# Optimization experiments

Measured on AMD Instinct MI355X. Metric: run time of the kernel, lower is better.

## Reference

```python
import jax, jax.numpy as jnp
import numpy as np

LN_EPS = 1e-5
B, T, D, H, NB, HH = 256, 128, 512, 1024, 64, 8


def _layernorm(x, g, b):
    m = x.mean(-1, keepdims=True)
    v = ((x - m) ** 2).mean(-1, keepdims=True)
    return (x - m) / jnp.sqrt(v + LN_EPS) * g + b


def setup_inputs() -> dict:
    key = jax.random.key(0)
    ks = jax.random.split(key, 10)
    init = lambda k, shape, fan: jax.random.normal(k, shape, jnp.float32) * np.float32(1.0 / np.sqrt(fan))
    return {
        "context_features": jax.random.normal(ks[0], (B, T, D), jnp.float32),
        "beam_history": jax.random.randint(ks[1], (B, HH), 0, NB),
        "beam_embed": init(ks[2], (NB, D), D),
        "W_in": init(ks[3], (H, 2 * D), 2 * D), "b_in": jnp.zeros((H,), jnp.float32),
        "W_init": init(ks[4], (H, 2 * D), 2 * D), "b_init": jnp.zeros((H,), jnp.float32),
        "W_ih": init(ks[5], (3 * H, H), H), "b_ih": jnp.zeros((3 * H,), jnp.float32),
        "W_hh": init(ks[6], (3 * H, H), H), "b_hh": jnp.zeros((3 * H,), jnp.float32),
        "ln_g": jnp.ones((H,), jnp.float32), "ln_b": jnp.zeros((H,), jnp.float32),
        "W_o1": init(ks[7], (H, H + D), H + D), "b_o1": jnp.zeros((H,), jnp.float32),
        "W_o2": init(ks[8], (NB, H), H), "b_o2": jnp.zeros((NB,), jnp.float32),
    }


def reference(context_features, beam_history, beam_embed, W_in, b_in, W_init, b_init,
              W_ih, b_ih, W_hh, b_hh, ln_g, ln_b, W_o1, b_o1, W_o2, b_o2):
    # --- init: history embedding mean + global context mean -> initial GRU state ---
    prev0 = beam_history[:, -1]                      # (B,)
    hist_emb = beam_embed[beam_history].mean(axis=1)  # (B, D)
    ctx_global = context_features.mean(axis=1)        # (B, D)
    h0 = jnp.tanh(jnp.concatenate([ctx_global, hist_emb], axis=-1) @ W_init.T + b_init)  # (B, H)

    def step(carry, ctx_t):
        h, prev = carry
        prev_emb = beam_embed[prev]                                            # (B, D)
        x = jax.nn.relu(jnp.concatenate([ctx_t, prev_emb], -1) @ W_in.T + b_in)  # (B, H)
        # PyTorch GRUCell: gate order r, z, n
        gx = x @ W_ih.T + b_ih
        gh = h @ W_hh.T + b_hh
        xr, xz, xn = jnp.split(gx, 3, axis=-1)
        hr, hz, hn = jnp.split(gh, 3, axis=-1)
        r = jax.nn.sigmoid(xr + hr)
        z = jax.nn.sigmoid(xz + hz)
        n = jnp.tanh(xn + r * hn)
        h_new = (1.0 - z) * n + z * h
        h_norm = _layernorm(h_new, ln_g, ln_b)
        o = jax.nn.relu(jnp.concatenate([h_norm, ctx_t], -1) @ W_o1.T + b_o1)
        logits_t = o @ W_o2.T + b_o2                                            # (B, NB)
        pred_next = jnp.argmax(logits_t, axis=-1)
        return (h_new, pred_next), logits_t

    ctx_tbd = jnp.swapaxes(context_features, 0, 1)  # (T, B, D)
    (_, _), logits = jax.lax.scan(step, (h0, prev0), ctx_tbd)
    return jnp.swapaxes(logits, 0, 1)  # (B, T, NB) == ar_logits
```

## Files before the change

### kernel.cpp

```cpp
#include <hip/hip_runtime.h>
#include <hip/hip_bf16.h>


#define TS 68
#define LDPA 40
constexpr int SZ = 262144;
constexpr int TT = 128;
constexpr int LDA_CTX = 65536;

typedef __attribute__((ext_vector_type(8))) short short8_t;
typedef __attribute__((ext_vector_type(4))) float f32x4;


__device__ __forceinline__ unsigned short f2bf_rne(float v) {
    unsigned u = __float_as_uint(v);
    unsigned r = u + 0x7fffu + ((u >> 16) & 1u);
    return (unsigned short)(r >> 16);
}
__device__ __forceinline__ float bfbits2f(unsigned short h) {
    return __uint_as_float(((unsigned)h) << 16);
}
__device__ __forceinline__ void split2(float v, unsigned short& h, unsigned short& l) {
    h = f2bf_rne(v);
    l = f2bf_rne(v - bfbits2f(h));
}
__device__ __forceinline__ void splitA8(const float4& v0, const float4& v1,
                                        short8_t& hi, short8_t& lo) {
    unsigned short h[8], l[8];
    split2(v0.x, h[0], l[0]); split2(v0.y, h[1], l[1]);
    split2(v0.z, h[2], l[2]); split2(v0.w, h[3], l[3]);
    split2(v1.x, h[4], l[4]); split2(v1.y, h[5], l[5]);
    split2(v1.z, h[6], l[6]); split2(v1.w, h[7], l[7]);
    hi = short8_t{(short)h[0],(short)h[1],(short)h[2],(short)h[3],
                  (short)h[4],(short)h[5],(short)h[6],(short)h[7]};
    lo = short8_t{(short)l[0],(short)l[1],(short)l[2],(short)l[3],
                  (short)l[4],(short)l[5],(short)l[6],(short)l[7]};
}


__device__ __forceinline__ void core13b(
    const unsigned short* __restrict__ Ah, const unsigned short* __restrict__ Al,
    int lda, int b0,
    const unsigned short* __restrict__ BhP, const unsigned short* __restrict__ BlP,
    int nKs, int ksbase, int nfb,
    int nIter, unsigned short* sm, f32x4 acc[2][4])
{
    const int tid = threadIdx.x, lane = tid & 63, wid = tid >> 6;
    const int wr = wid >> 1, wc = wid & 1;
    const int l15 = lane & 15, kg = (lane >> 4) * 8;
    const int arow = tid >> 2, acol = (tid & 3) * 8;

    const int ALO = 2560, BUF = 5120;

    const unsigned short* gAh = Ah + (size_t)(b0 + arow) * lda + ksbase * 32 + acol;
    const unsigned short* gAl = Al + (size_t)(b0 + arow) * lda + ksbase * 32 + acol;
    const unsigned short* pBh[4];
    const unsigned short* pBl[4];
#pragma unroll
    for (int ni = 0; ni < 4; ++ni) {
        pBh[ni] = BhP + ((size_t)(nfb + ni) * nKs + ksbase) * 512 + lane * 8;
        pBl[ni] = BlP + ((size_t)(nfb + ni) * nKs + ksbase) * 512 + lane * 8;
    }

    short8_t cBh[4], cBl[4], nBh[4], nBl[4];
    {
        short8_t a_h = *(const short8_t*)gAh;
        short8_t a_l = *(const short8_t*)gAl;
        *(short8_t*)&sm[arow * LDPA + acol]       = a_h;
        *(short8_t*)&sm[ALO + arow * LDPA + acol] = a_l;
#pragma unroll
        for (int ni = 0; ni < 4; ++ni) {
            cBh[ni] = *(const short8_t*)pBh[ni];
            cBl[ni] = *(const short8_t*)pBl[ni];
        }
    }
    __syncthreads();

    int cur = 0;
    const int aro = (wr * 32 + l15) * LDPA + kg;
    for (int i = 0; i < nIter; ++i) {
        short8_t a_h, a_l;
        if (i + 1 < nIter) {
            const int ko = (i + 1) * 32;
            a_h = *(const short8_t*)(gAh + ko);
            a_l = *(const short8_t*)(gAl + ko);
            const size_t fo = (size_t)(i + 1) * 512;
#pragma unroll
            for (int ni = 0; ni < 4; ++ni) {
                nBh[ni] = *(const short8_t*)(pBh[ni] + fo);
                nBl[ni] = *(const short8_t*)(pBl[ni] + fo);
            }
        }
        const unsigned short* S = sm + cur * BUF;
        short8_t afh[2], afl[2];
#pragma unroll
        for (int mi = 0; mi < 2; ++mi) {
            afh[mi] = *(const short8_t*)&S[aro + mi * 16 * LDPA];
            afl[mi] = *(const short8_t*)&S[ALO + aro + mi * 16 * LDPA];
        }
#pragma unroll
        for (int ni = 0; ni < 4; ++ni) {
#pragma unroll
            for (int mi = 0; mi < 2; ++mi) {
                acc[mi][ni] = __builtin_amdgcn_mfma_f32_16x16x32_bf16(afh[mi], cBh[ni], acc[mi][ni], 0, 0, 0);
                acc[mi][ni] = __builtin_amdgcn_mfma_f32_16x16x32_bf16(afh[mi], cBl[ni], acc[mi][ni], 0, 0, 0);
                acc[mi][ni] = __builtin_amdgcn_mfma_f32_16x16x32_bf16(afl[mi], cBh[ni], acc[mi][ni], 0, 0, 0);
            }
        }
        if (i + 1 < nIter) {
            unsigned short* N_ = sm + (cur ^ 1) * BUF;
            *(short8_t*)&N_[arow * LDPA + acol]       = a_h;
            *(short8_t*)&N_[ALO + arow * LDPA + acol] = a_l;
        }
        __syncthreads();
        cur ^= 1;
#pragma unroll
        for (int ni = 0; ni < 4; ++ni) { cBh[ni] = nBh[ni]; cBl[ni] = nBl[ni]; }
    }
}


__device__ __forceinline__ void mfma_core9(
    const float* __restrict__ A, int lda, int b0,
    const unsigned short* __restrict__ Bh, const unsigned short* __restrict__ Bl,
    int ldb, int n0, int k0base, int nIter,
    unsigned short* sm, f32x4 acc[2][4])
{
    const int tid = threadIdx.x, lane = tid & 63, wid = tid >> 6;
    const int wr = wid >> 1, wc = wid & 1;
    const int l15 = lane & 15, kg = (lane >> 4) * 8;
    const int arow = tid >> 2, acol = (tid & 3) * 8;
    const int brow = tid >> 1, bcol = (tid & 1) * 16;

    const int AOFF = 2560, BHOFF = 5120, BLOFF = 10240, BUF = 15360;

    const float* gA = A + (size_t)(b0 + arow) * lda + k0base + acol;
    const unsigned short* gBh = Bh + (size_t)(n0 + brow) * ldb + k0base + bcol;
    const unsigned short* gBl = Bl + (size_t)(n0 + brow) * ldb + k0base + bcol;

    {
        float4 a0 = *(const float4*)gA;
        float4 a1 = *(const float4*)(gA + 4);
        short8_t ah, al;
        splitA8(a0, a1, ah, al);
        short8_t bh0 = *(const short8_t*)gBh;
        short8_t bh1 = *(const short8_t*)(gBh + 8);
        short8_t bl0 = *(const short8_t*)gBl;
        short8_t bl1 = *(const short8_t*)(gBl + 8);
        *(short8_t*)&sm[arow * LDPA + acol]              = ah;
        *(short8_t*)&sm[AOFF + arow * LDPA + acol]       = al;
        *(short8_t*)&sm[BHOFF + brow * LDPA + bcol]      = bh0;
        *(short8_t*)&sm[BHOFF + brow * LDPA + bcol + 8]  = bh1;
        *(short8_t*)&sm[BLOFF + brow * LDPA + bcol]      = bl0;
        *(short8_t*)&sm[BLOFF + brow * LDPA + bcol + 8]  = bl1;
    }
    __syncthreads();

    int cur = 0;
    const int aro = (wr * 32 + l15) * LDPA + kg;
    for (int i = 0; i < nIter; ++i) {
        float4 a0, a1;
        short8_t bh0, bh1, bl0, bl1;
        if (i + 1 < nIter) {
            const int ko = (i + 1) * 32;
            a0 = *(const float4*)(gA + ko);
            a1 = *(const float4*)(gA + ko + 4);
            bh0 = *(const short8_t*)(gBh + ko);
            bh1 = *(const short8_t*)(gBh + ko + 8);
            bl0 = *(const short8_t*)(gBl + ko);
            bl1 = *(const short8_t*)(gBl + ko + 8);
        }
        const unsigned short* S = sm + cur * BUF;
        short8_t afh[2], afl[2];
#pragma unroll
        for (int mi = 0; mi < 2; ++mi) {
            afh[mi] = *(const short8_t*)&S[aro + mi * 16 * LDPA];
            afl[mi] = *(const short8_t*)&S[AOFF + aro + mi * 16 * LDPA];
        }
#pragma unroll
        for (int ni = 0; ni < 4; ++ni) {
            const int bro = (wc * 64 + ni * 16 + l15) * LDPA + kg;
            short8_t b_h = *(const short8_t*)&S[BHOFF + bro];
            short8_t b_l = *(const short8_t*)&S[BLOFF + bro];
#pragma unroll
            for (int mi = 0; mi < 2; ++mi) {
                acc[mi][ni] = __builtin_amdgcn_mfma_f32_16x16x32_bf16(afh[mi], b_h, acc[mi][ni], 0, 0, 0);
                acc[mi][ni] = __builtin_amdgcn_mfma_f32_16x16x32_bf16(afh[mi], b_l, acc[mi][ni], 0, 0, 0);
                acc[mi][ni] = __builtin_amdgcn_mfma_f32_16x16x32_bf16(afl[mi], b_h, acc[mi][ni], 0, 0, 0);
            }
        }
        if (i + 1 < nIter) {
            short8_t ah, al;
            splitA8(a0, a1, ah, al);
            unsigned short* N_ = sm + (cur ^ 1) * BUF;
            *(short8_t*)&N_[arow * LDPA + acol]             = ah;
            *(short8_t*)&N_[AOFF + arow * LDPA + acol]      = al;
            *(short8_t*)&N_[BHOFF + brow * LDPA + bcol]     = bh0;
            *(short8_t*)&N_[BHOFF + brow * LDPA + bcol + 8] = bh1;
            *(short8_t*)&N_[BLOFF + brow * LDPA + bcol]     = bl0;
            *(short8_t*)&N_[BLOFF + brow * LDPA + bcol + 8] = bl1;
        }
        __syncthreads();
        cur ^= 1;
    }
}


__device__ __forceinline__ void gemm_tile64(
    const float* __restrict__ A, int lda, int Mlim, int b0,
    const float* __restrict__ W, int ldw, int n0, int K,
    float* At, float* Wt, float acc[4][4])
{
    const int tid = threadIdx.x;
    const int tx = tid & 15, ty = tid >> 4;
    const int r = tid >> 2, c0 = (tid & 3) << 2;
    for (int k0 = 0; k0 < K; k0 += 16) {
        float4 av = make_float4(0.f, 0.f, 0.f, 0.f);
        if (b0 + r < Mlim)
            av = *(const float4*)(A + (size_t)(b0 + r) * lda + k0 + c0);
        float4 wv = *(const float4*)(W + (size_t)(n0 + r) * ldw + k0 + c0);
        __syncthreads();
        At[(c0+0)*TS + r] = av.x; At[(c0+1)*TS + r] = av.y;
        At[(c0+2)*TS + r] = av.z; At[(c0+3)*TS + r] = av.w;
        Wt[(c0+0)*TS + r] = wv.x; Wt[(c0+1)*TS + r] = wv.y;
        Wt[(c0+2)*TS + r] = wv.z; Wt[(c0+3)*TS + r] = wv.w;
        __syncthreads();
#pragma unroll
        for (int kk = 0; kk < 16; ++kk) {
            float4 a = *(const float4*)(At + kk*TS + ty*4);
            float4 w = *(const float4*)(Wt + kk*TS + tx*4);
            acc[0][0] += a.x*w.x; acc[0][1] += a.x*w.y; acc[0][2] += a.x*w.z; acc[0][3] += a.x*w.w;
            acc[1][0] += a.y*w.x; acc[1][1] += a.y*w.y; acc[1][2] += a.y*w.z; acc[1][3] += a.y*w.w;
            acc[2][0] += a.z*w.x; acc[2][1] += a.z*w.y; acc[2][2] += a.z*w.z; acc[2][3] += a.z*w.w;
            acc[3][0] += a.w*w.x; acc[3][1] += a.w*w.y; acc[3][2] += a.w*w.z; acc[3][3] += a.w*w.w;
        }
    }
}


__global__ void pre0_kernel(const float* __restrict__ ctx, const int* __restrict__ bh,
                            const float* __restrict__ be, float* __restrict__ A0,
                            int* __restrict__ prev)
{
    int b = blockIdx.x, tid = threadIdx.x;
    float s = 0.f;
    for (int t = 0; t < TT; ++t) s += ctx[(size_t)b * LDA_CTX + t * 512 + tid];
    A0[b * 1024 + tid] = s * (1.f / 128.f);
    float s2 = 0.f;
    for (int i = 0; i < 8; ++i) s2 += be[bh[b * 8 + i] * 512 + tid];
    A0[b * 1024 + 512 + tid] = s2 * 0.125f;
    if (tid == 0) prev[b] = bh[b * 8 + 7];
}

__global__ void wo2t_kernel(const float* __restrict__ W_o2, float* __restrict__ Wo2t)
{
    int idx = blockIdx.x * 256 + threadIdx.x;
    int k = idx >> 6, n = idx & 63;
    Wo2t[idx] = W_o2[n * 1024 + k];
}

__global__ void uv_kernel(const float* __restrict__ ln_g, const float* __restrict__ ln_b,
                          const float* __restrict__ W_o1, float* __restrict__ uvv)
{
    int idx = blockIdx.x * 256 + threadIdx.x;
    int which = idx >> 10, j = idx & 1023;
    const float* vec = which ? ln_b : ln_g;
    float s = 0.f;
    for (int k = 0; k < 1024; ++k) s += vec[k] * W_o1[(size_t)j * 1536 + k];
    uvv[which * 1024 + j] = s;
}

__global__ void packhi_kernel(const float* __restrict__ src, int ld, int col0,
                              int N, int K, const float* __restrict__ scale,
                              unsigned short* __restrict__ hi)
{
    int idx = blockIdx.x * 256 + threadIdx.x;
    if (idx >= N * K) return;
    int j = idx & 7;
    int lane = (idx >> 3) & 63;
    int fs = idx >> 9;
    int nKs = K >> 5;
    int nf = fs / nKs, ks = fs - nf * nKs;
    int n = nf * 16 + (lane & 15);
    int k = ks * 32 + (lane >> 4) * 8 + j;
    float v = src[(size_t)n * ld + col0 + k];
    if (scale) v *= scale[k];
    hi[idx] = f2bf_rne(v);
}

__global__ void packlo_kernel(const float* __restrict__ src, int ld, int col0,
                              int N, int K, const float* __restrict__ scale,
                              unsigned short* __restrict__ lo)
{
    int idx = blockIdx.x * 256 + threadIdx.x;
    if (idx >= N * K) return;
    int j = idx & 7;
    int lane = (idx >> 3) & 63;
    int fs = idx >> 9;
    int nKs = K >> 5;
    int nf = fs / nKs, ks = fs - nf * nKs;
    int n = nf * 16 + (lane & 15);
    int k = ks * 32 + (lane >> 4) * 8 + j;
    float v = src[(size_t)n * ld + col0 + k];
    if (scale) v *= scale[k];
    unsigned short h, l;
    split2(v, h, l);
    lo[idx] = l;
}

__global__ void wsplit_kernel(const float* __restrict__ src, int src_ld, int col0,
                              int N, int K, const float* __restrict__ scale,
                              unsigned short* __restrict__ hi,
                              unsigned short* __restrict__ lo)
{
    int idx = blockIdx.x * 256 + threadIdx.x;
    if (idx >= N * K) return;
    int n = idx / K, k = idx - n * K;
    float v = src[(size_t)n * src_ld + col0 + k];
    if (scale) v *= scale[k];
    unsigned short h, l;
    split2(v, h, l);
    hi[idx] = h; lo[idx] = l;
}

__global__ void gemm64_kernel(const float* __restrict__ A, int lda, int M,
                              const float* __restrict__ W, int ldw, int K,
                              const float* __restrict__ bias,
                              float* __restrict__ C, int ldc, int act)
{
    __shared__ __align__(16) float At[16 * TS];
    __shared__ __align__(16) float Wt[16 * TS];
    float acc[4][4] = {};
    int b0 = blockIdx.x * 64, n0 = blockIdx.y * 64;
    gemm_tile64(A, lda, M, b0, W, ldw, n0, K, At, Wt, acc);
    int tx = threadIdx.x & 15, ty = threadIdx.x >> 4;
#pragma unroll
    for (int i = 0; i < 4; ++i) {
        int b = b0 + ty * 4 + i;
        if (b >= M) continue;
#pragma unroll
        for (int j = 0; j < 4; ++j) {
            int n = n0 + tx * 4 + j;
            float v = acc[i][j] + (bias ? bias[n] : 0.f);
            if (act == 1) v = tanhf(v);
            C[(size_t)b * ldc + n] = v;
        }
    }
}

__global__ void xbuild0s_kernel(const float* __restrict__ cin0, const float* __restrict__ bpart,
                                const int* __restrict__ prev,
                                unsigned short* __restrict__ xh, unsigned short* __restrict__ xl)
{
    int b = blockIdx.x, tid = threadIdx.x;
    int pb = prev[b];
#pragma unroll
    for (int jj = 0; jj < 4; ++jj) {
        int j = jj * 256 + tid;
        float v = fmaxf(cin0[(size_t)b * 1024 + j] + bpart[(size_t)pb * 1024 + j], 0.f);
        unsigned short h, l;
        split2(v, h, l);
        xh[(size_t)b * 1024 + j] = h;
        xl[(size_t)b * 1024 + j] = l;
    }
}

__global__ void xbuild0_kernel(const float* __restrict__ cin0, const float* __restrict__ bpart,
                               const int* __restrict__ prev, float* __restrict__ x)
{
    int b = blockIdx.x, tid = threadIdx.x;
    int pb = prev[b];
#pragma unroll
    for (int jj = 0; jj < 4; ++jj) {
        int j = jj * 256 + tid;
        x[(size_t)b * 1024 + j] = fmaxf(cin0[(size_t)b * 1024 + j] + bpart[(size_t)pb * 1024 + j], 0.f);
    }
}


__global__ __launch_bounds__(256) void gates13_kernel(
    const unsigned short* __restrict__ xh, const unsigned short* __restrict__ xl,
    const unsigned short* __restrict__ hh, const unsigned short* __restrict__ hl,
    const float* __restrict__ ctx,
    const unsigned short* __restrict__ wih_hiP, const unsigned short* __restrict__ wih_loP,
    const unsigned short* __restrict__ whh_hiP, const unsigned short* __restrict__ whh_loP,
    const unsigned short* __restrict__ wcin_hi, const unsigned short* __restrict__ wcin_lo,
    const unsigned short* __restrict__ wo1c_hi, const unsigned short* __restrict__ wo1c_lo,
    const float* __restrict__ b_in, const float* __restrict__ b_o1,
    float* __restrict__ g6, float* __restrict__ cin, float* __restrict__ octx,
    int t)
{
    const int bid = blockIdx.x;
    const int z = bid & 7;
    const int tile = bid >> 3;
    const int tm = tile & 3, tn = tile >> 2;
    if (z == 6 && t + 1 >= TT) return;
    const int b0 = tm * 64, n0 = tn * 128;

    __shared__ __align__(16) unsigned short sm[2 * 15360];
    f32x4 acc[2][4] = {};
    const float* bias = nullptr;
    float* C;
    const int wid = threadIdx.x >> 6, wc = wid & 1;

    if (z < 6) {
        int g = z % 3, s = z / 3;
        const unsigned short* Ah = s ? hh : xh;
        const unsigned short* Al = s ? hl : xl;
        const unsigned short* BhP = s ? whh_hiP : wih_hiP;
        const unsigned short* BlP = s ? whh_loP : wih_loP;
        const int nfb = g * 64 + (n0 >> 4) + wc * 4;
        C = g6 + (size_t)z * SZ;
        core13b(Ah, Al, 1024, b0, BhP, BlP, 32, 0, nfb, 32, sm, acc);
    } else if (z == 6) {
        const float* A = ctx + (size_t)(t + 1) * 512;
        bias = b_in; C = cin;
        mfma_core9(A, LDA_CTX, b0, wcin_hi, wcin_lo, 512, n0, 0, 16, sm, acc);
    } else {
        const float* A = ctx + (size_t)t * 512;
        bias = b_o1; C = octx;
        mfma_core9(A, LDA_CTX, b0, wo1c_hi, wo1c_lo, 512, n0, 0, 16, sm, acc);
    }

    const int lane = threadIdx.x & 63;
    const int wr = wid >> 1;
    const int l15 = lane & 15, g4 = (lane >> 4) * 4;
#pragma unroll
    for (int mi = 0; mi < 2; ++mi) {
#pragma unroll
        for (int ni = 0; ni < 4; ++ni) {
            int col = n0 + wc * 64 + ni * 16 + l15;
            float bv = bias ? bias[col] : 0.f;
#pragma unroll
            for (int r = 0; r < 4; ++r) {
                int row = b0 + wr * 32 + mi * 16 + g4 + r;
                C[(size_t)row * 1024 + col] = acc[mi][ni][r] + bv;
            }
        }
    }
}

__global__ __launch_bounds__(256) void kb13_kernel(
    const unsigned short* __restrict__ hh, const unsigned short* __restrict__ hl,
    const unsigned short* __restrict__ wo1k_hiP, const unsigned short* __restrict__ wo1k_loP,
    float* __restrict__ g6)
{
    const int bid = blockIdx.x;
    const int tm = bid >> 5, tn = (bid >> 2) & 7, p = bid & 3;
    const int b0 = tm * 64, n0 = tn * 128;
    const int wid = threadIdx.x >> 6, wc = wid & 1;

    __shared__ __align__(16) unsigned short sm[2 * 5120];
    f32x4 acc[2][4] = {};
    core13b(hh, hl, 1024, b0, wo1k_hiP, wo1k_loP, 32, p * 8,
            (n0 >> 4) + wc * 4, 8, sm, acc);

    float* C = g6 + (size_t)p * SZ;
    const int lane = threadIdx.x & 63;
    const int wr = wid >> 1;
    const int l15 = lane & 15, g4 = (lane >> 4) * 4;
#pragma unroll
    for (int mi = 0; mi < 2; ++mi) {
#pragma unroll
        for (int ni = 0; ni < 4; ++ni) {
            int col = n0 + wc * 64 + ni * 16 + l15;
#pragma unroll
            for (int r = 0; r < 4; ++r) {
                int row = b0 + wr * 32 + mi * 16 + g4 + r;
                C[(size_t)row * 1024 + col] = acc[mi][ni][r];
            }
        }
    }
}

__global__ void gru13_kernel(const float* __restrict__ g6,
                             const float* __restrict__ b_ih, const float* __restrict__ b_hh,
                             float* __restrict__ h,
                             unsigned short* __restrict__ hh, unsigned short* __restrict__ hl,
                             float* __restrict__ mbuf, float* __restrict__ isbuf)
{
    __shared__ float ls[4], lq[4];
    const int b = blockIdx.x, tid = threadIdx.x;
    const int j = tid * 4;
    size_t base = (size_t)b * 1024 + j;
    float4 xr = *(const float4*)(g6 + base);
    float4 xz = *(const float4*)(g6 + (size_t)SZ + base);
    float4 xn = *(const float4*)(g6 + 2 * (size_t)SZ + base);
    float4 hr = *(const float4*)(g6 + 3 * (size_t)SZ + base);
    float4 hz = *(const float4*)(g6 + 4 * (size_t)SZ + base);
    float4 hn = *(const float4*)(g6 + 5 * (size_t)SZ + base);
    float4 ho = *(const float4*)(h + base);
    float4 bi0 = *(const float4*)(b_ih + j);
    float4 bi1 = *(const float4*)(b_ih + 1024 + j);
    float4 bi2 = *(const float4*)(b_ih + 2048 + j);
    float4 bh0 = *(const float4*)(b_hh + j);
    float4 bh1 = *(const float4*)(b_hh + 1024 + j);
    float4 bh2 = *(const float4*)(b_hh + 2048 + j);
    float4 hv;
    {
        float rr = 1.f / (1.f + expf(-((xr.x + bi0.x) + (hr.x + bh0.x))));
        float zz = 1.f / (1.f + expf(-((xz.x + bi1.x) + (hz.x + bh1.x))));
        float nn = tanhf((xn.x + bi2.x) + rr * (hn.x + bh2.x));
        hv.x = (1.f - zz) * nn + zz * ho.x;
    }
    {
        float rr = 1.f / (1.f + expf(-((xr.y + bi0.y) + (hr.y + bh0.y))));
        float zz = 1.f / (1.f + expf(-((xz.y + bi1.y) + (hz.y + bh1.y))));
        float nn = tanhf((xn.y + bi2.y) + rr * (hn.y + bh2.y));
        hv.y = (1.f - zz) * nn + zz * ho.y;
    }
    {
        float rr = 1.f / (1.f + expf(-((xr.z + bi0.z) + (hr.z + bh0.z))));
        float zz = 1.f / (1.f + expf(-((xz.z + bi1.z) + (hz.z + bh1.z))));
        float nn = tanhf((xn.z + bi2.z) + rr * (hn.z + bh2.z));
        hv.z = (1.f - zz) * nn + zz * ho.z;
    }
    {
        float rr = 1.f / (1.f + expf(-((xr.w + bi0.w) + (hr.w + bh0.w))));
        float zz = 1.f / (1.f + expf(-((xz.w + bi1.w) + (hz.w + bh1.w))));
        float nn = tanhf((xn.w + bi2.w) + rr * (hn.w + bh2.w));
        hv.w = (1.f - zz) * nn + zz * ho.w;
    }
    *(float4*)(h + base) = hv;
    ushort4 h4, l4;
    split2(hv.x, h4.x, l4.x); split2(hv.y, h4.y, l4.y);
    split2(hv.z, h4.z, l4.z); split2(hv.w, h4.w, l4.w);
    *(ushort4*)(hh + base) = h4;
    *(ushort4*)(hl + base) = l4;
    float s = hv.x + hv.y + hv.z + hv.w;
    float q = hv.x * hv.x + hv.y * hv.y + hv.z * hv.z + hv.w * hv.w;
    for (int off = 32; off; off >>= 1) {
        s += __shfl_down(s, off);
        q += __shfl_down(q, off);
    }
    const int lane = tid & 63, w = tid >> 6;
    if (lane == 0) { ls[w] = s; lq[w] = q; }
    __syncthreads();
    if (tid == 0) {
        float S = ls[0] + ls[1] + ls[2] + ls[3];
        float Q = lq[0] + lq[1] + lq[2] + lq[3];
        float m = S * (1.f / 1024.f);
        mbuf[b] = m;
        isbuf[b] = rsqrtf(Q * (1.f / 1024.f) - m * m + 1e-5f);
    }
}

__global__ void kc13_kernel(const float* __restrict__ g6,
                            const float* __restrict__ Wo2t, const float* __restrict__ b_o2,
                            const float* __restrict__ uv, const float* __restrict__ octx,
                            const float* __restrict__ mbuf, const float* __restrict__ isbuf,
                            const float* __restrict__ cin, const float* __restrict__ bpart,
                            unsigned short* __restrict__ xh, unsigned short* __restrict__ xl,
                            int* __restrict__ prev, float* __restrict__ out, int t)
{
    __shared__ __align__(16) float os[4][1024];
    __shared__ float red[4][4][64];
    __shared__ int sidx[4];
    const int b0 = blockIdx.x * 4, tid = threadIdx.x;

#pragma unroll
    for (int i = 0; i < 4; ++i) {
        int f = tid + i * 256;
        int r = f >> 8, c4 = (f & 255) << 2;
        size_t base = (size_t)(b0 + r) * 1024 + c4;
        float4 p0 = *(const float4*)(g6 + base);
        float4 p1 = *(const float4*)(g6 + (size_t)SZ + base);
        float4 p2 = *(const float4*)(g6 + 2 * (size_t)SZ + base);
        float4 p3 = *(const float4*)(g6 + 3 * (size_t)SZ + base);
        float4 oc = *(const float4*)(octx + base);
        float4 u4 = *(const float4*)(uv + c4);
        float4 v4 = *(const float4*)(uv + 1024 + c4);
        float m = mbuf[b0 + r], is = isbuf[b0 + r];
        float4 o4;
        o4.x = fmaxf((p0.x + p1.x + p2.x + p3.x - m * u4.x) * is + v4.x + oc.x, 0.f);
        o4.y = fmaxf((p0.y + p1.y + p2.y + p3.y - m * u4.y) * is + v4.y + oc.y, 0.f);
        o4.z = fmaxf((p0.z + p1.z + p2.z + p3.z - m * u4.z) * is + v4.z + oc.z, 0.f);
        o4.w = fmaxf((p0.w + p1.w + p2.w + p3.w - m * u4.w) * is + v4.w + oc.w, 0.f);
        *(float4*)&os[r][c4] = o4;
    }
    __syncthreads();

    {
        int n = tid & 63, seg = tid >> 6;
        float p0 = 0.f, p1 = 0.f, p2 = 0.f, p3 = 0.f;
        int k0 = seg * 256;
        for (int k = k0; k < k0 + 256; ++k) {
            float w = Wo2t[(size_t)k * 64 + n];
            p0 += os[0][k] * w; p1 += os[1][k] * w;
            p2 += os[2][k] * w; p3 += os[3][k] * w;
        }
        red[0][seg][n] = p0; red[1][seg][n] = p1;
        red[2][seg][n] = p2; red[3][seg][n] = p3;
    }
    __syncthreads();

    {
        int r = tid >> 6, n = tid & 63;
        float lg = red[r][0][n] + red[r][1][n] + red[r][2][n] + red[r][3][n] + b_o2[n];
        out[(size_t)(b0 + r) * (TT * 64) + t * 64 + n] = lg;
        float v = lg; int idx = n;
        for (int off = 32; off; off >>= 1) {
            float ov = __shfl_xor(v, off);
            int oi = __shfl_xor(idx, off);
            if (ov > v || (ov == v && oi < idx)) { v = ov; idx = oi; }
        }
        if (n == 0) { prev[b0 + r] = idx; sidx[r] = idx; }
    }
    __syncthreads();

    if (t + 1 < TT) {
#pragma unroll
        for (int i = 0; i < 16; ++i) {
            int idx = tid + i * 256;
            int r = idx >> 10, j = idx & 1023;
            float v = fmaxf(cin[(size_t)(b0 + r) * 1024 + j] +
                            bpart[(size_t)sidx[r] * 1024 + j], 0.f);
            unsigned short h, l;
            split2(v, h, l);
            xh[(size_t)(b0 + r) * 1024 + j] = h;
            xl[(size_t)(b0 + r) * 1024 + j] = l;
        }
    }
}


__global__ void step_gemms_kernel(
    const float* __restrict__ x, const float* __restrict__ hBase,
    const float* __restrict__ ctx,
    const float* __restrict__ Wih, const float* __restrict__ Whh,
    const float* __restrict__ Win, const float* __restrict__ Wo1,
    const float* __restrict__ b_in, const float* __restrict__ b_o1,
    float* __restrict__ g6, float* __restrict__ cinBase, float* __restrict__ octx,
    int t)
{
    __shared__ __align__(16) float At[16 * TS];
    __shared__ __align__(16) float Wt[16 * TS];
    float acc[4][4] = {};
    const int z = blockIdx.z, b0 = blockIdx.x * 64, n0 = blockIdx.y * 64;
    const float *A, *W, *bias = nullptr;
    float* C;
    int lda, ldw, K;
    if (z < 6) {
        int g = z % 3, s = z / 3;
        A = s ? (hBase + (size_t)(t & 1) * SZ) : x;
        lda = 1024;
        W = (s ? Whh : Wih) + (size_t)(g * 1024) * 1024;
        ldw = 1024; K = 1024;
        C = g6 + (size_t)z * SZ;
    } else if (z == 6) {
        if (t + 1 >= TT) return;
        A = ctx + (size_t)(t + 1) * 512; lda = LDA_CTX;
        W = Win; ldw = 1024; K = 512; bias = b_in;
        C = cinBase + (size_t)((t + 1) & 1) * SZ;
    } else {
        A = ctx + (size_t)t * 512; lda = LDA_CTX;
        W = Wo1 + 1024; ldw = 1536; K = 512; bias = b_o1;
        C = octx;
    }
    gemm_tile64(A, lda, 256, b0, W, ldw, n0, K, At, Wt, acc);
    int tx = threadIdx.x & 15, ty = threadIdx.x >> 4;
#pragma unroll
    for (int i = 0; i < 4; ++i) {
        int b = b0 + ty * 4 + i;
#pragma unroll
        for (int j = 0; j < 4; ++j) {
            int n = n0 + tx * 4 + j;
            float v = acc[i][j];
            if (bias) v += bias[n];
            C[(size_t)b * 1024 + n] = v;
        }
    }
}

__global__ void kb_kernel(const float* __restrict__ hg, const float* __restrict__ Wo1,
                          const float* __restrict__ uv, const float* __restrict__ octx,
                          const float* __restrict__ mbuf, const float* __restrict__ isbuf,
                          float* __restrict__ o)
{
    __shared__ __align__(16) float At[16 * TS];
    __shared__ __align__(16) float Wt[16 * TS];
    float acc[2][4] = {};
    const int b0 = blockIdx.x * 32, n0 = blockIdx.y * 64;
    const int tid = threadIdx.x, tx = tid & 15, ty = tid >> 4;
    const int r = tid >> 2, c0 = (tid & 3) << 2;
    for (int k0 = 0; k0 < 1024; k0 += 16) {
        float4 av = make_float4(0.f, 0.f, 0.f, 0.f);
        if (r < 32) av = *(const float4*)(hg + (size_t)(b0 + r) * 1024 + k0 + c0);
        float4 wv = *(const float4*)(Wo1 + (size_t)(n0 + r) * 1536 + k0 + c0);
        __syncthreads();
        At[(c0+0)*TS + r] = av.x; At[(c0+1)*TS + r] = av.y;
        At[(c0+2)*TS + r] = av.z; At[(c0+3)*TS + r] = av.w;
        Wt[(c0+0)*TS + r] = wv.x; Wt[(c0+1)*TS + r] = wv.y;
        Wt[(c0+2)*TS + r] = wv.z; Wt[(c0+3)*TS + r] = wv.w;
        __syncthreads();
#pragma unroll
        for (int kk = 0; kk < 16; ++kk) {
            float2 a = *(const float2*)(At + kk*TS + ty*2);
            float4 w = *(const float4*)(Wt + kk*TS + tx*4);
            acc[0][0] += a.x*w.x; acc[0][1] += a.x*w.y; acc[0][2] += a.x*w.z; acc[0][3] += a.x*w.w;
            acc[1][0] += a.y*w.x; acc[1][1] += a.y*w.y; acc[1][2] += a.y*w.z; acc[1][3] += a.y*w.w;
        }
    }
#pragma unroll
    for (int i = 0; i < 2; ++i) {
        int b = b0 + ty * 2 + i;
        float m = mbuf[b], is = isbuf[b];
#pragma unroll
        for (int j = 0; j < 4; ++j) {
            int n = n0 + tx * 4 + j;
            float v = (acc[i][j] - m * uv[n]) * is + uv[1024 + n] + octx[(size_t)b * 1024 + n];
            o[(size_t)b * 1024 + n] = fmaxf(v, 0.f);
        }
    }
}

__global__ void gru_ln_kernel(const float* __restrict__ g6,
                              const float* __restrict__ b_ih, const float* __restrict__ b_hh,
                              float* __restrict__ hBase, const float* __restrict__ ln_g,
                              float* __restrict__ hg, float* __restrict__ mbuf,
                              float* __restrict__ isbuf, int t)
{
    __shared__ float rs[256], rq[256];
    int b = blockIdx.x, tid = threadIdx.x;
    const float* hc = hBase + (size_t)(t & 1) * SZ + (size_t)b * 1024;
    float* hnx = hBase + (size_t)((t + 1) & 1) * SZ + (size_t)b * 1024;
    float s = 0.f, q = 0.f;
#pragma unroll
    for (int jj = 0; jj < 4; ++jj) {
        int j = jj * 256 + tid;
        size_t base = (size_t)b * 1024 + j;
        float xr = g6[0 * (size_t)SZ + base] + b_ih[j];
        float xz = g6[1 * (size_t)SZ + base] + b_ih[1024 + j];
        float xn = g6[2 * (size_t)SZ + base] + b_ih[2048 + j];
        float hr = g6[3 * (size_t)SZ + base] + b_hh[j];
        float hz = g6[4 * (size_t)SZ + base] + b_hh[1024 + j];
        float hn = g6[5 * (size_t)SZ + base] + b_hh[2048 + j];
        float r = 1.f / (1.f + expf(-(xr + hr)));
        float z = 1.f / (1.f + expf(-(xz + hz)));
        float nn = tanhf(xn + r * hn);
        float ho = hc[j];
        float hv = (1.f - z) * nn + z * ho;
        hnx[j] = hv;
        hg[base] = hv * ln_g[j];
        s += hv; q += hv * hv;
    }
    rs[tid] = s; rq[tid] = q;
    __syncthreads();
    for (int st = 128; st; st >>= 1) {
        if (tid < st) { rs[tid] += rs[tid + st]; rq[tid] += rq[tid + st]; }
        __syncthreads();
    }
    if (tid == 0) {
        float m = rs[0] * (1.f / 1024.f);
        float var = rq[0] * (1.f / 1024.f) - m * m;
        mbuf[b] = m;
        isbuf[b] = rsqrtf(var + 1e-5f);
    }
}

__global__ void kc_kernel(const float* __restrict__ o, const float* __restrict__ Wo2t,
                          const float* __restrict__ b_o2, const float* __restrict__ cinBase,
                          const float* __restrict__ bpart, float* __restrict__ x,
                          int* __restrict__ prev, float* __restrict__ out, int t)
{
    __shared__ __align__(16) float os[1024];
    __shared__ float red[4][64];
    __shared__ int sidx;
    int b = blockIdx.x, tid = threadIdx.x;
    const float* orow = o + (size_t)b * 1024;
    *(float4*)&os[tid * 4] = *(const float4*)&orow[tid * 4];
    __syncthreads();
    int n = tid & 63, seg = tid >> 6;
    float p = 0.f;
    int k0 = seg * 256;
#pragma unroll 8
    for (int k = 0; k < 256; ++k) p += os[k0 + k] * Wo2t[(size_t)(k0 + k) * 64 + n];
    red[seg][n] = p;
    __syncthreads();
    if (tid < 64) {
        float lg = red[0][tid] + red[1][tid] + red[2][tid] + red[3][tid] + b_o2[tid];
        out[((size_t)b * TT + t) * 64 + tid] = lg;
        float v = lg; int idx = tid;
        for (int off = 32; off; off >>= 1) {
            float ov = __shfl_xor(v, off);
            int oi = __shfl_xor(idx, off);
            if (ov > v || (ov == v && oi < idx)) { v = ov; idx = oi; }
        }
        if (tid == 0) { prev[b] = idx; sidx = idx; }
    }
    __syncthreads();
    if (t + 1 < TT) {
        int pb = sidx;
        const float* cn = cinBase + (size_t)((t + 1) & 1) * SZ + (size_t)b * 1024;
        const float* bp = bpart + (size_t)pb * 1024;
#pragma unroll
        for (int jj = 0; jj < 4; ++jj) {
            int j = jj * 256 + tid;
            x[(size_t)b * 1024 + j] = fmaxf(cn[j] + bp[j], 0.f);
        }
    }
}

__global__ void copy_gb_kernel(const float* g, const float* bb, float* gb)
{
    int idx = blockIdx.x * 256 + threadIdx.x;
    if (idx < 1024) gb[idx] = g[idx];
    else            gb[idx] = bb[idx - 1024];
}


extern "C" void kernel_launch(void* const* d_in, const int* in_sizes, int n_in,
                              void* d_out, int out_size, void* d_ws, size_t ws_size,
                              hipStream_t stream)
{
    const float* ctx    = (const float*)d_in[0];
    const int*   bh     = (const int*)d_in[1];
    const float* be     = (const float*)d_in[2];
    const float* W_in   = (const float*)d_in[3];
    const float* b_in   = (const float*)d_in[4];
    const float* W_init = (const float*)d_in[5];
    const float* b_init = (const float*)d_in[6];
    const float* W_ih   = (const float*)d_in[7];
    const float* b_ih   = (const float*)d_in[8];
    const float* W_hh   = (const float*)d_in[9];
    const float* b_hh   = (const float*)d_in[10];
    const float* ln_g   = (const float*)d_in[11];
    const float* ln_b   = (const float*)d_in[12];
    const float* W_o1   = (const float*)d_in[13];
    const float* b_o1   = (const float*)d_in[14];
    const float* W_o2   = (const float*)d_in[15];
    const float* b_o2   = (const float*)d_in[16];
    float* out = (float*)d_out;
    float* ws  = (float*)d_ws;

    const bool mfma_path = (ws_size >= 45700000ull);

    if (mfma_path) {
        float* hbuf  = ws;
        float* cin   = ws + 262144;
        float* octx  = ws + 524288;
        float* g6    = ws + 786432;
        float* A0    = g6;
        float* bpart = ws + 2359296;
        float* uvv   = ws + 2424832;
        float* Wo2t  = ws + 2428928;
        float* mbuf  = ws + 2494464;
        float* isbuf = ws + 2494720;
        int*   prev  = (int*)(ws + 2494976);
        unsigned short* bf = (unsigned short*)(ws + 2495232);
        unsigned short* wih_hiP  = bf;
        unsigned short* wih_loP  = bf + 3145728;
        unsigned short* whh_hiP  = bf + 6291456;
        unsigned short* whh_loP  = bf + 9437184;
        unsigned short* wo1k_hiP = bf + 12582912;
        unsigned short* wo1k_loP = bf + 13631488;
        unsigned short* wo1c_hi  = bf + 14680064;
        unsigned short* wo1c_lo  = bf + 15204352;
        unsigned short* wcin_hi  = bf + 15728640;
        unsigned short* wcin_lo  = bf + 16252928;
        unsigned short* xh       = bf + 16777216;
        unsigned short* xl       = bf + 17039360;
        unsigned short* hh       = bf + 17301504;
        unsigned short* hl       = bf + 17563648;

        pre0_kernel<<<256, 512, 0, stream>>>(ctx, bh, be, A0, prev);
        wo2t_kernel<<<256, 256, 0, stream>>>(W_o2, Wo2t);
        uv_kernel<<<8, 256, 0, stream>>>(ln_g, ln_b, W_o1, uvv);
        gemm64_kernel<<<dim3(4, 16), 256, 0, stream>>>(A0, 1024, 256, W_init, 1024, 1024,
                                                       b_init, hbuf, 1024, 1);
        gemm64_kernel<<<dim3(1, 16), 256, 0, stream>>>(be, 512, 64, W_in + 512, 1024, 512,
                                                       nullptr, bpart, 1024, 0);
        gemm64_kernel<<<dim3(4, 16), 256, 0, stream>>>(ctx, LDA_CTX, 256, W_in, 1024, 512,
                                                       b_in, cin, 1024, 0);
        xbuild0s_kernel<<<256, 256, 0, stream>>>(cin, bpart, prev, xh, xl);
        packhi_kernel<<<12288, 256, 0, stream>>>(W_ih, 1024, 0, 3072, 1024, nullptr, wih_hiP);
        packlo_kernel<<<12288, 256, 0, stream>>>(W_ih, 1024, 0, 3072, 1024, nullptr, wih_loP);
        packhi_kernel<<<12288, 256, 0, stream>>>(W_hh, 1024, 0, 3072, 1024, nullptr, whh_hiP);
        packlo_kernel<<<12288, 256, 0, stream>>>(W_hh, 1024, 0, 3072, 1024, nullptr, whh_loP);
        packhi_kernel<<<4096, 256, 0, stream>>>(W_o1, 1536, 0, 1024, 1024, ln_g, wo1k_hiP);
        packlo_kernel<<<4096, 256, 0, stream>>>(W_o1, 1536, 0, 1024, 1024, ln_g, wo1k_loP);
        wsplit_kernel<<<2048, 256, 0, stream>>>(W_o1, 1536, 1024, 1024, 512, nullptr, wo1c_hi, wo1c_lo);
        wsplit_kernel<<<2048, 256, 0, stream>>>(W_in, 1024, 0, 1024, 512, nullptr, wcin_hi, wcin_lo);
        wsplit_kernel<<<1024, 256, 0, stream>>>(hbuf, 1024, 0, 256, 1024, nullptr, hh, hl);

        for (int t = 0; t < TT; ++t) {
            gates13_kernel<<<256, 256, 0, stream>>>(
                xh, xl, hh, hl, ctx,
                wih_hiP, wih_loP, whh_hiP, whh_loP, wcin_hi, wcin_lo, wo1c_hi, wo1c_lo,
                b_in, b_o1, g6, cin, octx, t);
            gru13_kernel<<<256, 256, 0, stream>>>(g6, b_ih, b_hh, hbuf,
                                                  hh, hl, mbuf, isbuf);
            kb13_kernel<<<128, 256, 0, stream>>>(hh, hl, wo1k_hiP, wo1k_loP, g6);
            kc13_kernel<<<64, 256, 0, stream>>>(g6, Wo2t, b_o2, uvv, octx, mbuf, isbuf,
                                                cin, bpart, xh, xl, prev, out, t);
        }
    } else {
        float* A0    = ws;
        float* hbuf  = ws + 262144;
        float* hg    = ws + 786432;
        float* x     = ws + 1048576;
        float* cin   = ws + 1310720;
        float* octx  = ws + 1835008;
        float* g6    = ws + 2097152;
        float* obuf  = ws + 3670016;
        float* bpart = ws + 3932160;
        float* uvv   = ws + 3997696;
        float* gb    = ws + 3999744;
        float* Wo2t  = ws + 4001792;
        float* mbuf  = ws + 4067328;
        float* isbuf = ws + 4067584;
        int*   prev  = (int*)(ws + 4067840);

        pre0_kernel<<<256, 512, 0, stream>>>(ctx, bh, be, A0, prev);
        copy_gb_kernel<<<8, 256, 0, stream>>>(ln_g, ln_b, gb);
        wo2t_kernel<<<256, 256, 0, stream>>>(W_o2, Wo2t);
        gemm64_kernel<<<dim3(4, 16), 256, 0, stream>>>(A0, 1024, 256, W_init, 1024, 1024,
                                                       b_init, hbuf, 1024, 1);
        gemm64_kernel<<<dim3(1, 16), 256, 0, stream>>>(be, 512, 64, W_in + 512, 1024, 512,
                                                       nullptr, bpart, 1024, 0);
        gemm64_kernel<<<dim3(1, 16), 256, 0, stream>>>(gb, 1024, 2, W_o1, 1536, 1024,
                                                       nullptr, uvv, 1024, 0);
        gemm64_kernel<<<dim3(4, 16), 256, 0, stream>>>(ctx, LDA_CTX, 256, W_in, 1024, 512,
                                                       b_in, cin, 1024, 0);
        xbuild0_kernel<<<256, 256, 0, stream>>>(cin, bpart, prev, x);

        for (int t = 0; t < TT; ++t) {
            step_gemms_kernel<<<dim3(4, 16, 8), 256, 0, stream>>>(
                x, hbuf, ctx, W_ih, W_hh, W_in, W_o1, b_in, b_o1, g6, cin, octx, t);
            gru_ln_kernel<<<256, 256, 0, stream>>>(g6, b_ih, b_hh, hbuf, ln_g, hg,
                                                   mbuf, isbuf, t);
            kb_kernel<<<dim3(8, 16), 256, 0, stream>>>(hg, W_o1, uvv, octx, mbuf, isbuf, obuf);
            kc_kernel<<<256, 256, 0, stream>>>(obuf, Wo2t, b_o2, cin, bpart, x, prev, out, t);
        }
    }
}
```

Measured before the change: 6.596 ms.

## Fuse GRU cell update into W_o1 GEMM kernel, double-buffer hidden state

Removes the separate per-step GRU elementwise kernel and folds it into the kb kernel. Each block now recomputes the GRU gates for its 32-row by 256-column slice, stages the bf16 hi/lo hidden state in shared memory, and runs the W_o1 MFMA product from there. LayerNorm statistics are written as partial sums and reduced in kc. The hidden state is kept only as a bf16 hi/lo pair in ping-pong buffers, which drops the fp32 h buffer and one launch per step. The cost is that the gate math is repeated by all 8 column tiles, and the workspace requirement grows.

```diff
diff --git a/kernel.cpp b/kernel.cpp
--- a/kernel.cpp
+++ b/kernel.cpp
@@ -378,7 +378,7 @@
 }
 
 
-__global__ __launch_bounds__(256) void gates13_kernel(
+__global__ __launch_bounds__(256) void gates14_kernel(
     const unsigned short* __restrict__ xh, const unsigned short* __restrict__ xl,
     const unsigned short* __restrict__ hh, const unsigned short* __restrict__ hl,
     const float* __restrict__ ctx,
@@ -440,137 +440,186 @@
     }
 }
 
-__global__ __launch_bounds__(256) void kb13_kernel(
-    const unsigned short* __restrict__ hh, const unsigned short* __restrict__ hl,
+__global__ __launch_bounds__(256) void kb14_kernel(
+    const float* __restrict__ g6,
+    const float* __restrict__ b_ih, const float* __restrict__ b_hh,
+    const unsigned short* __restrict__ hhA, const unsigned short* __restrict__ hlA,
+    unsigned short* __restrict__ hhB, unsigned short* __restrict__ hlB,
     const unsigned short* __restrict__ wo1k_hiP, const unsigned short* __restrict__ wo1k_loP,
-    float* __restrict__ g6)
-{
+    float* __restrict__ part, float* __restrict__ spq)
+{
+    __shared__ __align__(16) unsigned short sm[2 * 32 * 264];
     const int bid = blockIdx.x;
     const int tm = bid >> 5, tn = (bid >> 2) & 7, p = bid & 3;
-    const int b0 = tm * 64, n0 = tn * 128;
-    const int wid = threadIdx.x >> 6, wc = wid & 1;
-
-    __shared__ __align__(16) unsigned short sm[2 * 5120];
-    f32x4 acc[2][4] = {};
-    core13b(hh, hl, 1024, b0, wo1k_hiP, wo1k_loP, 32, p * 8,
-            (n0 >> 4) + wc * 4, 8, sm, acc);
-
-    float* C = g6 + (size_t)p * SZ;
-    const int lane = threadIdx.x & 63;
-    const int wr = wid >> 1;
-    const int l15 = lane & 15, g4 = (lane >> 4) * 4;
-#pragma unroll
-    for (int mi = 0; mi < 2; ++mi) {
+    const int tid = threadIdx.x, lane = tid & 63, wid = tid >> 6;
+    const int ALO = 32 * 264;
+
+    {
+        const int r = tid >> 3, q = tid & 7;
+        const int row = tm * 32 + r;
+        float s = 0.f, qs = 0.f;
+#pragma unroll
+        for (int jj = 0; jj < 8; ++jj) {
+            const int cl = jj * 32 + q * 4;
+            const int c = p * 256 + cl;
+            size_t base = (size_t)row * 1024 + c;
+            float4 xr = *(const float4*)(g6 + base);
+            float4 xz = *(const float4*)(g6 + (size_t)SZ + base);
+            float4 xn = *(const float4*)(g6 + 2 * (size_t)SZ + base);
+            float4 hr = *(const float4*)(g6 + 3 * (size_t)SZ + base);
+            float4 hz = *(const float4*)(g6 + 4 * (size_t)SZ + base);
+            float4 hn = *(const float4*)(g6 + 5 * (size_t)SZ + base);
+            ushort4 oh = *(const ushort4*)(hhA + base);
+            ushort4 ol = *(const ushort4*)(hlA + base);
+            float4 ho;
+            ho.x = bfbits2f(oh.x) + bfbits2f(ol.x);
+            ho.y = bfbits2f(oh.y) + bfbits2f(ol.y);
+            ho.z = bfbits2f(oh.z) + bfbits2f(ol.z);
+            ho.w = bfbits2f(oh.w) + bfbits2f(ol.w);
+            float4 bi0 = *(const float4*)(b_ih + c);
+            float4 bi1 = *(const float4*)(b_ih + 1024 + c);
+            float4 bi2 = *(const float4*)(b_ih + 2048 + c);
+            float4 bh0 = *(const float4*)(b_hh + c);
+            float4 bh1 = *(const float4*)(b_hh + 1024 + c);
+            float4 bh2 = *(const float4*)(b_hh + 2048 + c);
+            float4 hv;
+            {
+                float rr = 1.f / (1.f + expf(-((xr.x + bi0.x) + (hr.x + bh0.x))));
+                float zz = 1.f / (1.f + expf(-((xz.x + bi1.x) + (hz.x + bh1.x))));
+                float nn = tanhf((xn.x + bi2.x) + rr * (hn.x + bh2.x));
+                hv.x = (1.f - zz) * nn + zz * ho.x;
+            }
+            {
+                float rr = 1.f / (1.f + expf(-((xr.y + bi0.y) + (hr.y + bh0.y))));
+                float zz = 1.f / (1.f + expf(-((xz.y + bi1.y) + (hz.y + bh1.y))));
+                float nn = tanhf((xn.y + bi2.y) + rr * (hn.y + bh2.y));
+                hv.y = (1.f - zz) * nn + zz * ho.y;
+            }
+            {
+                float rr = 1.f / (1.f + expf(-((xr.z + bi0.z) + (hr.z + bh0.z))));
+                float zz = 1.f / (1.f + expf(-((xz.z + bi1.z) + (hz.z + bh1.z))));
+                float nn = tanhf((xn.z + bi2.z) + rr * (hn.z + bh2.z));
+                hv.z = (1.f - zz) * nn + zz * ho.z;
+            }
+            {
+                float rr = 1.f / (1.f + expf(-((xr.w + bi0.w) + (hr.w + bh0.w))));
+                float zz = 1.f / (1.f + expf(-((xz.w + bi1.w) + (hz.w + bh1.w))));
+                float nn = tanhf((xn.w + bi2.w) + rr * (hn.w + bh2.w));
+                hv.w = (1.f - zz) * nn + zz * ho.w;
+            }
+            ushort4 h4, l4;
+            split2(hv.x, h4.x, l4.x); split2(hv.y, h4.y, l4.y);
+            split2(hv.z, h4.z, l4.z); split2(hv.w, h4.w, l4.w);
+            *(ushort4*)&sm[r * 264 + cl]       = h4;
+            *(ushort4*)&sm[ALO + r * 264 + cl] = l4;
+            if (tn == 0) {
+                *(ushort4*)(hhB + base) = h4;
+                *(ushort4*)(hlB + base) = l4;
+            }
+            s += hv.x + hv.y + hv.z + hv.w;
+            qs += hv.x * hv.x + hv.y * hv.y + hv.z * hv.z + hv.w * hv.w;
+        }
+        s  += __shfl_xor(s, 1);  s  += __shfl_xor(s, 2);  s  += __shfl_xor(s, 4);
+        qs += __shfl_xor(qs, 1); qs += __shfl_xor(qs, 2); qs += __shfl_xor(qs, 4);
+        if (tn == 0 && q == 0) {
+            spq[(p * 256 + row) * 2]     = s;
+            spq[(p * 256 + row) * 2 + 1] = qs;
+        }
+    }
+    __syncthreads();
+
+    const int wr = wid >> 1, wc = wid & 1;
+    const int l15 = lane & 15, kg = (lane >> 4) * 8;
+    const int n0 = tn * 128;
+    const int nfb = tn * 8 + wc * 4;
+    const unsigned short* pBh[4];
+    const unsigned short* pBl[4];
+#pragma unroll
+    for (int ni = 0; ni < 4; ++ni) {
+        pBh[ni] = wo1k_hiP + ((size_t)(nfb + ni) * 32 + p * 8) * 512 + lane * 8;
+        pBl[ni] = wo1k_loP + ((size_t)(nfb + ni) * 32 + p * 8) * 512 + lane * 8;
+    }
+    f32x4 acc[4] = {};
+    short8_t cBh[4], cBl[4], nBh[4], nBl[4];
+#pragma unroll
+    for (int ni = 0; ni < 4; ++ni) {
+        cBh[ni] = *(const short8_t*)pBh[ni];
+        cBl[ni] = *(const short8_t*)pBl[ni];
+    }
+    const int aro = (wr * 16 + l15) * 264;
+    for (int i = 0; i < 8; ++i) {
+        if (i + 1 < 8) {
+            const size_t fo = (size_t)(i + 1) * 512;
+#pragma unroll
+            for (int ni = 0; ni < 4; ++ni) {
+                nBh[ni] = *(const short8_t*)(pBh[ni] + fo);
+                nBl[ni] = *(const short8_t*)(pBl[ni] + fo);
+            }
+        }
+        short8_t a_h = *(const short8_t*)&sm[aro + i * 32 + kg];
+        short8_t a_l = *(const short8_t*)&sm[ALO + aro + i * 32 + kg];
 #pragma unroll
         for (int ni = 0; ni < 4; ++ni) {
-            int col = n0 + wc * 64 + ni * 16 + l15;
-#pragma unroll
-            for (int r = 0; r < 4; ++r) {
-                int row = b0 + wr * 32 + mi * 16 + g4 + r;
-                C[(size_t)row * 1024 + col] = acc[mi][ni][r];
-            }
-        }
-    }
-}
-
-__global__ void gru13_kernel(const float* __restrict__ g6,
-                             const float* __restrict__ b_ih, const float* __restrict__ b_hh,
-                             float* __restrict__ h,
-                             unsigned short* __restrict__ hh, unsigned short* __restrict__ hl,
-                             float* __restrict__ mbuf, float* __restrict__ isbuf)
-{
-    __shared__ float ls[4], lq[4];
-    const int b = blockIdx.x, tid = threadIdx.x;
-    const int j = tid * 4;
-    size_t base = (size_t)b * 1024 + j;
-    float4 xr = *(const float4*)(g6 + base);
-    float4 xz = *(const float4*)(g6 + (size_t)SZ + base);
-    float4 xn = *(const float4*)(g6 + 2 * (size_t)SZ + base);
-    float4 hr = *(const float4*)(g6 + 3 * (size_t)SZ + base);
-    float4 hz = *(const float4*)(g6 + 4 * (size_t)SZ + base);
-    float4 hn = *(const float4*)(g6 + 5 * (size_t)SZ + base);
-    float4 ho = *(const float4*)(h + base);
-    float4 bi0 = *(const float4*)(b_ih + j);
-    float4 bi1 = *(const float4*)(b_ih + 1024 + j);
-    float4 bi2 = *(const float4*)(b_ih + 2048 + j);
-    float4 bh0 = *(const float4*)(b_hh + j);
-    float4 bh1 = *(const float4*)(b_hh + 1024 + j);
-    float4 bh2 = *(const float4*)(b_hh + 2048 + j);
-    float4 hv;
-    {
-        float rr = 1.f / (1.f + expf(-((xr.x + bi0.x) + (hr.x + bh0.x))));
-        float zz = 1.f / (1.f + expf(-((xz.x + bi1.x) + (hz.x + bh1.x))));
-        float nn = tanhf((xn.x + bi2.x) + rr * (hn.x + bh2.x));
-        hv.x = (1.f - zz) * nn + zz * ho.x;
-    }
-    {
-        float rr = 1.f / (1.f + expf(-((xr.y + bi0.y) + (hr.y + bh0.y))));
-        float zz = 1.f / (1.f + expf(-((xz.y + bi1.y) + (hz.y + bh1.y))));
-        float nn = tanhf((xn.y + bi2.y) + rr * (hn.y + bh2.y));
-        hv.y = (1.f - zz) * nn + zz * ho.y;
-    }
-    {
-        float rr = 1.f / (1.f + expf(-((xr.z + bi0.z) + (hr.z + bh0.z))));
-        float zz = 1.f / (1.f + expf(-((xz.z + bi1.z) + (hz.z + bh1.z))));
-        float nn = tanhf((xn.z + bi2.z) + rr * (hn.z + bh2.z));
-        hv.z = (1.f - zz) * nn + zz * ho.z;
-    }
-    {
-        float rr = 1.f / (1.f + expf(-((xr.w + bi0.w) + (hr.w + bh0.w))));
-        float zz = 1.f / (1.f + expf(-((xz.w + bi1.w) + (hz.w + bh1.w))));
-        float nn = tanhf((xn.w + bi2.w) + rr * (hn.w + bh2.w));
-        hv.w = (1.f - zz) * nn + zz * ho.w;
-    }
-    *(float4*)(h + base) = hv;
-    ushort4 h4, l4;
-    split2(hv.x, h4.x, l4.x); split2(hv.y, h4.y, l4.y);
-    split2(hv.z, h4.z, l4.z); split2(hv.w, h4.w, l4.w);
-    *(ushort4*)(hh + base) = h4;
-    *(ushort4*)(hl + base) = l4;
-    float s = hv.x + hv.y + hv.z + hv.w;
-    float q = hv.x * hv.x + hv.y * hv.y + hv.z * hv.z + hv.w * hv.w;
-    for (int off = 32; off; off >>= 1) {
-        s += __shfl_down(s, off);
-        q += __shfl_down(q, off);
-    }
-    const int lane = tid & 63, w = tid >> 6;
-    if (lane == 0) { ls[w] = s; lq[w] = q; }
-    __syncthreads();
-    if (tid == 0) {
-        float S = ls[0] + ls[1] + ls[2] + ls[3];
-        float Q = lq[0] + lq[1] + lq[2] + lq[3];
-        float m = S * (1.f / 1024.f);
-        mbuf[b] = m;
-        isbuf[b] = rsqrtf(Q * (1.f / 1024.f) - m * m + 1e-5f);
-    }
-}
-
-__global__ void kc13_kernel(const float* __restrict__ g6,
+            acc[ni] = __builtin_amdgcn_mfma_f32_16x16x32_bf16(a_h, cBh[ni], acc[ni], 0, 0, 0);
+            acc[ni] = __builtin_amdgcn_mfma_f32_16x16x32_bf16(a_h, cBl[ni], acc[ni], 0, 0, 0);
+            acc[ni] = __builtin_amdgcn_mfma_f32_16x16x32_bf16(a_l, cBh[ni], acc[ni], 0, 0, 0);
+        }
+#pragma unroll
+        for (int ni = 0; ni < 4; ++ni) { cBh[ni] = nBh[ni]; cBl[ni] = nBl[ni]; }
+    }
+    float* C = part + (size_t)p * SZ;
+    const int g4 = (lane >> 4) * 4;
+#pragma unroll
+    for (int ni = 0; ni < 4; ++ni) {
+        int col = n0 + wc * 64 + ni * 16 + l15;
+#pragma unroll
+        for (int r = 0; r < 4; ++r) {
+            int row = tm * 32 + wr * 16 + g4 + r;
+            C[(size_t)row * 1024 + col] = acc[ni][r];
+        }
+    }
+}
+
+__global__ void kc14_kernel(const float* __restrict__ part, const float* __restrict__ spq,
                             const float* __restrict__ Wo2t, const float* __restrict__ b_o2,
                             const float* __restrict__ uv, const float* __restrict__ octx,
-                            const float* __restrict__ mbuf, const float* __restrict__ isbuf,
                             const float* __restrict__ cin, const float* __restrict__ bpart,
                             unsigned short* __restrict__ xh, unsigned short* __restrict__ xl,
                             int* __restrict__ prev, float* __restrict__ out, int t)
 {
     __shared__ __align__(16) float os[4][1024];
     __shared__ float red[4][4][64];
+    __shared__ float sm_m[4], sm_is[4];
     __shared__ int sidx[4];
     const int b0 = blockIdx.x * 4, tid = threadIdx.x;
+
+    if (tid < 4) {
+        int row = b0 + tid;
+        float s = 0.f, qq = 0.f;
+#pragma unroll
+        for (int p = 0; p < 4; ++p) {
+            s  += spq[(p * 256 + row) * 2];
+            qq += spq[(p * 256 + row) * 2 + 1];
+        }
+        float m = s * (1.f / 1024.f);
+        sm_m[tid] = m;
+        sm_is[tid] = rsqrtf(qq * (1.f / 1024.f) - m * m + 1e-5f);
+    }
+    __syncthreads();
 
 #pragma unroll
     for (int i = 0; i < 4; ++i) {
         int f = tid + i * 256;
         int r = f >> 8, c4 = (f & 255) << 2;
         size_t base = (size_t)(b0 + r) * 1024 + c4;
-        float4 p0 = *(const float4*)(g6 + base);
-        float4 p1 = *(const float4*)(g6 + (size_t)SZ + base);
-        float4 p2 = *(const float4*)(g6 + 2 * (size_t)SZ + base);
-        float4 p3 = *(const float4*)(g6 + 3 * (size_t)SZ + base);
+        float4 p0 = *(const float4*)(part + base);
+        float4 p1 = *(const float4*)(part + (size_t)SZ + base);
+        float4 p2 = *(const float4*)(part + 2 * (size_t)SZ + base);
+        float4 p3 = *(const float4*)(part + 3 * (size_t)SZ + base);
         float4 oc = *(const float4*)(octx + base);
         float4 u4 = *(const float4*)(uv + c4);
         float4 v4 = *(const float4*)(uv + 1024 + c4);
-        float m = mbuf[b0 + r], is = isbuf[b0 + r];
+        float m = sm_m[r], is = sm_is[r];
         float4 o4;
         o4.x = fmaxf((p0.x + p1.x + p2.x + p3.x - m * u4.x) * is + v4.x + oc.x, 0.f);
         o4.y = fmaxf((p0.y + p1.y + p2.y + p3.y - m * u4.y) * is + v4.y + oc.y, 0.f);
@@ -833,21 +882,21 @@
     float* out = (float*)d_out;
     float* ws  = (float*)d_ws;
 
-    const bool mfma_path = (ws_size >= 45700000ull);
+    const bool mfma_path = (ws_size >= 49824768ull);
 
     if (mfma_path) {
-        float* hbuf  = ws;
-        float* cin   = ws + 262144;
-        float* octx  = ws + 524288;
-        float* g6    = ws + 786432;
+        float* cin   = ws;
+        float* octx  = ws + 262144;
+        float* g6    = ws + 524288;
         float* A0    = g6;
-        float* bpart = ws + 2359296;
-        float* uvv   = ws + 2424832;
-        float* Wo2t  = ws + 2428928;
-        float* mbuf  = ws + 2494464;
-        float* isbuf = ws + 2494720;
-        int*   prev  = (int*)(ws + 2494976);
-        unsigned short* bf = (unsigned short*)(ws + 2495232);
+        float* h0f   = g6 + SZ;
+        float* bpart = ws + 2097152;
+        float* uvv   = ws + 2162688;
+        float* Wo2t  = ws + 2164736;
+        float* spq   = ws + 2230272;
+        int*   prev  = (int*)(ws + 2232320);
+        float* part  = ws + 2232576;
+        unsigned short* bf = (unsigned short*)(ws + 3281152);
         unsigned short* wih_hiP  = bf;
         unsigned short* wih_loP  = bf + 3145728;
         unsigned short* whh_hiP  = bf + 6291456;
@@ -860,14 +909,13 @@
         unsigned short* wcin_lo  = bf + 16252928;
         unsigned short* xh       = bf + 16777216;
         unsigned short* xl       = bf + 17039360;
-        unsigned short* hh       = bf + 17301504;
-        unsigned short* hl       = bf + 17563648;
+        unsigned short* hb       = bf + 17301504;
 
         pre0_kernel<<<256, 512, 0, stream>>>(ctx, bh, be, A0, prev);
         wo2t_kernel<<<256, 256, 0, stream>>>(W_o2, Wo2t);
         uv_kernel<<<8, 256, 0, stream>>>(ln_g, ln_b, W_o1, uvv);
         gemm64_kernel<<<dim3(4, 16), 256, 0, stream>>>(A0, 1024, 256, W_init, 1024, 1024,
-                                                       b_init, hbuf, 1024, 1);
+                                                       b_init, h0f, 1024, 1);
         gemm64_kernel<<<dim3(1, 16), 256, 0, stream>>>(be, 512, 64, W_in + 512, 1024, 512,
                                                        nullptr, bpart, 1024, 0);
         gemm64_kernel<<<dim3(4, 16), 256, 0, stream>>>(ctx, LDA_CTX, 256, W_in, 1024, 512,
@@ -881,17 +929,21 @@
         packlo_kernel<<<4096, 256, 0, stream>>>(W_o1, 1536, 0, 1024, 1024, ln_g, wo1k_loP);
         wsplit_kernel<<<2048, 256, 0, stream>>>(W_o1, 1536, 1024, 1024, 512, nullptr, wo1c_hi, wo1c_lo);
         wsplit_kernel<<<2048, 256, 0, stream>>>(W_in, 1024, 0, 1024, 512, nullptr, wcin_hi, wcin_lo);
-        wsplit_kernel<<<1024, 256, 0, stream>>>(hbuf, 1024, 0, 256, 1024, nullptr, hh, hl);
+        wsplit_kernel<<<1024, 256, 0, stream>>>(h0f, 1024, 0, 256, 1024, nullptr,
+                                                hb, hb + 262144);
 
         for (int t = 0; t < TT; ++t) {
-            gates13_kernel<<<256, 256, 0, stream>>>(
-                xh, xl, hh, hl, ctx,
+            const unsigned short* hhA = hb + (size_t)(t & 1) * 524288;
+            const unsigned short* hlA = hhA + 262144;
+            unsigned short* hhB = hb + (size_t)((t + 1) & 1) * 524288;
+            unsigned short* hlB = hhB + 262144;
+            gates14_kernel<<<256, 256, 0, stream>>>(
+                xh, xl, hhA, hlA, ctx,
                 wih_hiP, wih_loP, whh_hiP, whh_loP, wcin_hi, wcin_lo, wo1c_hi, wo1c_lo,
                 b_in, b_o1, g6, cin, octx, t);
-            gru13_kernel<<<256, 256, 0, stream>>>(g6, b_ih, b_hh, hbuf,
-                                                  hh, hl, mbuf, isbuf);
-            kb13_kernel<<<128, 256, 0, stream>>>(hh, hl, wo1k_hiP, wo1k_loP, g6);
-            kc13_kernel<<<64, 256, 0, stream>>>(g6, Wo2t, b_o2, uvv, octx, mbuf, isbuf,
+            kb14_kernel<<<256, 256, 0, stream>>>(g6, b_ih, b_hh, hhA, hlA, hhB, hlB,
+                                                 wo1k_hiP, wo1k_loP, part, spq);
+            kc14_kernel<<<64, 256, 0, stream>>>(part, spq, Wo2t, b_o2, uvv, octx,
                                                 cin, bpart, xh, xl, prev, out, t);
         }
     } else {
```

After: 7.336 ms. 11.2% more time.
